# Optimization experiments

Measured on AMD Instinct MI355X. Metric: run time of the kernel, lower is better.

The kernel has to match this reference:

```python
import jax, jax.numpy as jnp
import numpy as np

NUM_HEADS = 8
EPS = 1e-12  # torch F.normalize eps


def setup_inputs() -> dict:
    key = jax.random.key(0)
    k1, k2, k3 = jax.random.split(key, 3)
    B, N, C = 8, 4096, 768
    x = jax.random.normal(k1, (B, N, C), dtype=jnp.float32)
    Wqkv = jax.random.normal(k2, (C, 3 * C), dtype=jnp.float32) * 0.02
    temperature = jnp.ones((NUM_HEADS, 1, 1), dtype=jnp.float32)
    Wproj = jax.random.normal(k3, (C, C), dtype=jnp.float32) * 0.02
    bproj = jnp.zeros((C,), dtype=jnp.float32)
    return {"x": x, "Wqkv": Wqkv, "temperature": temperature,
            "Wproj": Wproj, "bproj": bproj}


def _l2norm(t):
    # torch F.normalize(dim=-1): x / max(||x||, eps)
    n = jnp.sqrt(jnp.sum(t * t, axis=-1, keepdims=True))
    return t / jnp.maximum(n, EPS)


def reference(x, Wqkv, temperature, Wproj, bproj):
    B, N, C = x.shape
    H = NUM_HEADS
    Ch = C // H
    qkv = (x @ Wqkv).reshape(B, N, 3, H, Ch)
    qkv = qkv.transpose(2, 0, 3, 1, 4)           # (3, B, H, N, Ch)
    q, k, v = qkv[0], qkv[1], qkv[2]
    # transpose(-2,-1): attend over channels -> (B, H, Ch, N)
    q = jnp.swapaxes(q, -2, -1)
    k = jnp.swapaxes(k, -2, -1)
    v = jnp.swapaxes(v, -2, -1)
    q = _l2norm(q)
    k = _l2norm(k)
    # (B, H, Ch, Ch) channel-attention scores, scaled by learned temperature
    attn = jnp.einsum('bhcn,bhdn->bhcd', q, k) * temperature
    attn = jax.nn.softmax(attn, axis=-1)
    out = jnp.einsum('bhcd,bhdn->bhcn', attn, v)  # (B, H, Ch, N)
    out = out.transpose(0, 3, 1, 2).reshape(B, N, C)
    return out @ Wproj + bproj
```

## Files before the change

### kernel.cpp

```cpp
#include <hip/hip_runtime.h>
#include <cstdint>
#include <cstddef>

typedef unsigned short u16;
typedef short bf16x8 __attribute__((ext_vector_type(8)));
typedef unsigned short u16x4 __attribute__((ext_vector_type(4)));
typedef unsigned short u16x8 __attribute__((ext_vector_type(8)));
typedef float f32x4 __attribute__((ext_vector_type(4)));

#define EPSN 1e-12f

__device__ __forceinline__ u16 f2bf(float f) {
  uint32_t u = __builtin_bit_cast(uint32_t, f);
  u += 0x7FFFu + ((u >> 16) & 1u);
  return (u16)(u >> 16);
}
__device__ __forceinline__ float bf2f(u16 h) {
  uint32_t u = ((uint32_t)h) << 16;
  return __builtin_bit_cast(float, u);
}

__device__ __forceinline__ void gll16(const u16* g, u16* l) {
  __builtin_amdgcn_global_load_lds(
      (const __attribute__((address_space(1))) void*)g,
      (__attribute__((address_space(3))) void*)l, 16, 0, 0);
}

__global__ __launch_bounds__(256)
void k_cvtT(const float* __restrict__ x, u16* __restrict__ Xh,
            u16* __restrict__ XhT) {
  __shared__ u16 tr[64][68];
  const int tid = threadIdx.x;
  const int t0 = blockIdx.x * 64, k0 = blockIdx.y * 64, b = blockIdx.z;
  const int rq = tid >> 4;
  const int cq = tid & 15;
  const size_t base = ((size_t)b * 4096 + t0) * 768 + k0;
  u16 m[4][4];
#pragma unroll
  for (int e = 0; e < 4; e++) {
    const int r = rq * 4 + e;
    f32x4 v = *(const f32x4*)(x + base + (size_t)r * 768 + cq * 4);
    u16x4 o;
#pragma unroll
    for (int q = 0; q < 4; q++) o[q] = f2bf(v[q]);
    *(u16x4*)(Xh + base + (size_t)r * 768 + cq * 4) = o;
    m[e][0] = o[0]; m[e][1] = o[1]; m[e][2] = o[2]; m[e][3] = o[3];
  }
#pragma unroll
  for (int q = 0; q < 4; q++) {
    u16x4 w;
    w[0] = m[0][q]; w[1] = m[1][q]; w[2] = m[2][q]; w[3] = m[3][q];
    *(u16x4*)&tr[cq * 4 + q][rq * 4] = w;
  }
  __syncthreads();
  const size_t tbase = ((size_t)b * 768 + k0) * 4096 + t0;
#pragma unroll
  for (int p = 0; p < 4; p++) {
    const int kk = (tid >> 4) + p * 16;
    const int ts = (tid & 15) * 4;
    u16x4 o = *(const u16x4*)&tr[kk][ts];
    *(u16x4*)(XhT + tbase + (size_t)kk * 4096 + ts) = o;
  }
}

__global__ __launch_bounds__(256)
void k_wt(const float* __restrict__ W, u16* __restrict__ Wt, u16* __restrict__ Wvh) {
  __shared__ float tile[32][33];
  const int j0 = blockIdx.x * 32;
  const int k0 = blockIdx.y * 32;
  const int tx = threadIdx.x & 31;
  const int ty = threadIdx.x >> 5;
#pragma unroll
  for (int r = 0; r < 4; r++) {
    float v = W[(size_t)(k0 + ty + r * 8) * 2304 + j0 + tx];
    tile[ty + r * 8][tx] = v;
    if (j0 >= 1536)
      Wvh[(size_t)(k0 + ty + r * 8) * 768 + (j0 - 1536) + tx] = f2bf(v);
  }
  __syncthreads();
  if (j0 < 1536) {
#pragma unroll
    for (int r = 0; r < 4; r++)
      Wt[(size_t)(j0 + ty + r * 8) * 768 + k0 + tx] = f2bf(tile[tx][ty + r * 8]);
  }
}

template <int OUTF32B, int TRI>
__global__ __launch_bounds__(256, 3)
void k_gemm(const u16* __restrict__ A, const u16* __restrict__ Btp,
            void* __restrict__ Cp, const float* __restrict__ bias,
            int K, int lda, int ldb, int ldc,
            long aZ, long bZ, long cZ, int zK, long kss) {
  const int gx = gridDim.x, gy = gridDim.y;
  int f = blockIdx.x + gx * (blockIdx.y + gy * blockIdx.z);
  const int total = gx * gy * gridDim.z;
  const int q = total >> 3, rr = total & 7;
  const int xcd = f & 7, kk0 = f >> 3;
  f = (xcd < rr ? xcd * (q + 1) : rr * (q + 1) + (xcd - rr) * q) + kk0;
  const int bx = f % gx;
  const int tmp = f / gx;
  const int by = tmp % gy;
  const int bz = tmp / gy;

  int m0, n0;
  if constexpr (TRI) {
    const int ty = (bx >= 20) ? 5 : (bx >= 18) ? 4 : (bx >= 15) ? 3
                 : (bx >= 11) ? 2 : (bx >= 6) ? 1 : 0;
    const int txi = ty + (bx - (ty * 6 - (ty * (ty - 1)) / 2));
    m0 = ty * 128;
    n0 = txi * 128;
  } else {
    m0 = by * 128;
    n0 = bx * 128;
  }
  const int z = bz;
  const int bb = z / zK, ss = z % zK;
  const u16* Az = A + (long)bb * aZ + (long)ss * kss;
  const u16* Btz = Btp + (long)bb * bZ + (long)ss * kss;

  __shared__ u16 As[3 * 128 * 32];
  __shared__ u16 Bs[3 * 128 * 32];
  const int tid = threadIdx.x;
  const int lane = tid & 63;
  const int wid = tid >> 6;
  const int wr = wid >> 1, wc = wid & 1;
  const int fm = lane & 15, kg = lane >> 4;

  const int lr = lane >> 2;
  const int gk = (lane & 3) ^ ((lane >> 3) & 3);
  const u16* gA = Az + (size_t)(m0 + wid * 32 + lr) * lda + gk * 8;
  const u16* gB = Btz + (size_t)(n0 + wid * 32 + lr) * ldb + gk * 8;
  const size_t a16 = (size_t)16 * lda, b16 = (size_t)16 * ldb;
  u16* lA = As + wid * 1024;
  u16* lB = Bs + wid * 1024;
  const int kq = (kg ^ ((fm >> 1) & 3)) * 8;

  auto STAGE = [&](int slot, int ko) {
    u16* la = lA + slot * 4096;
    u16* lb = lB + slot * 4096;
    gll16(gA + ko, la);
    gll16(gA + ko + a16, la + 512);
    gll16(gB + ko, lb);
    gll16(gB + ko + b16, lb + 512);
  };

  const int nt = K >> 5;
  STAGE(0, 0);
  STAGE(1, 32);
  int sl = 0;

  f32x4 acc[4][4] = {};
  for (int t = 0; t < nt; ++t) {
    if (t + 1 < nt) {
      asm volatile("s_waitcnt vmcnt(4)" ::: "memory");
    } else {
      asm volatile("s_waitcnt vmcnt(0)" ::: "memory");
    }
    __builtin_amdgcn_sched_barrier(0);
    __builtin_amdgcn_s_barrier();
    __builtin_amdgcn_sched_barrier(0);

    if (t + 2 < nt) {
      int s2 = sl + 2; if (s2 >= 3) s2 -= 3;
      STAGE(s2, (t + 2) * 32);
    }

    const u16* as_ = As + sl * 4096;
    const u16* bs_ = Bs + sl * 4096;
    bf16x8 af[4], bfr[4];
#pragma unroll
    for (int i = 0; i < 4; i++)
      af[i] = *(const bf16x8*)&as_[(wr * 64 + i * 16 + fm) * 32 + kq];
#pragma unroll
    for (int j = 0; j < 4; j++)
      bfr[j] = *(const bf16x8*)&bs_[(wc * 64 + j * 16 + fm) * 32 + kq];
    asm volatile("s_waitcnt lgkmcnt(0)" ::: "memory");
    __builtin_amdgcn_sched_barrier(0);

#pragma unroll
    for (int i = 0; i < 4; i++)
#pragma unroll
      for (int j = 0; j < 4; j++)
        acc[i][j] = __builtin_amdgcn_mfma_f32_16x16x32_bf16(af[i], bfr[j], acc[i][j], 0, 0, 0);

    sl++; if (sl == 3) sl = 0;
  }

  if constexpr (OUTF32B) {
    float* C = (float*)Cp + (long)z * cZ;
#pragma unroll
    for (int j = 0; j < 4; j++) {
      const int col = n0 + wc * 64 + j * 16 + fm;
      const float bj = bias[col];
#pragma unroll
      for (int i = 0; i < 4; i++) {
        const int r0 = m0 + wr * 64 + i * 16 + kg * 4;
#pragma unroll
        for (int r = 0; r < 4; r++)
          C[(size_t)(r0 + r) * ldc + col] = acc[i][j][r] + bj;
      }
    }
  } else {
    const int rb = TRI ? 0 : m0;
    const int cb = TRI ? 0 : n0;
    const int ld = TRI ? 128 : ldc;
    u16* C = (u16*)Cp + (long)z * cZ + (TRI ? (long)bx * 16384 : 0L);
#pragma unroll
    for (int j = 0; j < 4; j++) {
      const int col = cb + wc * 64 + j * 16 + fm;
#pragma unroll
      for (int i = 0; i < 4; i++) {
        const int r0 = rb + wr * 64 + i * 16 + kg * 4;
#pragma unroll
        for (int r = 0; r < 4; r++)
          C[(size_t)(r0 + r) * ld + col] = f2bf(acc[i][j][r]);
      }
    }
  }
}

__global__ __launch_bounds__(256)
void k_red(const u16* __restrict__ P, u16* __restrict__ O) {
  const int b = blockIdx.y;
  const int ti = blockIdx.x / 6, tj = blockIdx.x % 6;
  const bool mirror = ti > tj;
  const int a = mirror ? tj : ti;
  const int c2 = mirror ? ti : tj;
  const int src = a * 6 - (a * (a - 1)) / 2 + (c2 - a);
  __shared__ u16 lt[128 * 128];
  const int tid = threadIdx.x;
  const int r = tid >> 1;
  const int ch = (tid & 1) * 64;
  float acc[64] = {};
  for (int s = 0; s < 4; s++) {
    const u16* p = P + ((size_t)(b * 4 + s) * 344064 + (size_t)src * 16384);
    __syncthreads();
#pragma unroll
    for (int it = 0; it < 8; it++) {
      const int idx = (tid + it * 256) * 8;
      *(u16x8*)&lt[idx] = *(const u16x8*)(p + idx);
    }
    __syncthreads();
    if (!mirror) {
#pragma unroll
      for (int e = 0; e < 64; e++) acc[e] += bf2f(lt[r * 128 + ch + e]);
    } else {
#pragma unroll
      for (int e = 0; e < 64; e++) acc[e] += bf2f(lt[(ch + e) * 128 + r]);
    }
  }
  u16* o = O + (size_t)b * 589824 + (size_t)(ti * 128 + r) * 768 + tj * 128 + ch;
#pragma unroll
  for (int v8 = 0; v8 < 8; v8++) {
    u16x8 w;
#pragma unroll
    for (int e = 0; e < 8; e++) w[e] = f2bf(acc[v8 * 8 + e]);
    *(u16x8*)(o + v8 * 8) = w;
  }
}

__global__ __launch_bounds__(256)
void k_score(const u16* __restrict__ Tm, const u16* __restrict__ Wt,
             const float* __restrict__ temperature, float* __restrict__ Aattn) {
  const int h = blockIdx.x, b = blockIdx.y;
  const int bh = b * 8 + h;
  __shared__ u16 As[96 * 32];
  __shared__ u16 Bs[96 * 32];
  __shared__ u16 Dt2[96 * 32];
  __shared__ u16 Dwq[96 * 32];
  __shared__ float Gs[96 * 96];
  __shared__ float nqs[96], nks[96], invk[96];

  const int tid = threadIdx.x;
  const int lane = tid & 63;
  const int wid = tid >> 6;
  const int wr = wid >> 1, wc = wid & 1;
  const int fm = lane & 15, kg = lane >> 4;
  const int lr = lane >> 2;
  const int gkS = (lane & 3) ^ ((lane >> 3) & 3);
  const int gkL = (lane & 3);
  const int kq = (kg ^ ((fm >> 1) & 3)) * 8;

  const u16* baseT1 = Tm + (size_t)b * 1179648 + (size_t)(h * 96) * 768;
  const u16* baseT2 = baseT1 + (size_t)768 * 768;
  const u16* baseWq = Wt + (size_t)(h * 96) * 768;
  const u16* baseWk = baseWq + (size_t)768 * 768;

  const u16* gsrc;
  u16* ldst;
  int gblk = gkS;
  if (wid == 0) { gsrc = baseT1; ldst = As; }
  else if (wid == 1) { gsrc = baseWk; ldst = Bs; }
  else if (wid == 2) { gsrc = baseT2; ldst = Dt2; gblk = gkL; }
  else { gsrc = baseWq; ldst = Dwq; gblk = gkL; }

  f32x4 acc[3][3] = {};
  float nqa = 0.f, nka = 0.f;
  const int sw1 = (tid < 96) ? ((tid >> 1) & 3) : 0;
  const int sw2 = (tid >= 128 && tid < 224) ? (((tid - 128) >> 1) & 3) : 0;

  for (int k0 = 0; k0 < 768; k0 += 32) {
    __syncthreads();
#pragma unroll
    for (int c = 0; c < 6; c++) {
      gll16(gsrc + (size_t)(c * 16 + lr) * 768 + k0 + gblk * 8,
            ldst + c * 512);
    }
    __syncthreads();
    bf16x8 af[3], bfr[3];
#pragma unroll
    for (int i = 0; i < 3; i++)
      af[i] = *(const bf16x8*)&As[(wr * 48 + i * 16 + fm) * 32 + kq];
#pragma unroll
    for (int j = 0; j < 3; j++)
      bfr[j] = *(const bf16x8*)&Bs[(wc * 48 + j * 16 + fm) * 32 + kq];
#pragma unroll
    for (int i = 0; i < 3; i++)
#pragma unroll
      for (int j = 0; j < 3; j++)
        acc[i][j] = __builtin_amdgcn_mfma_f32_16x16x32_bf16(af[i], bfr[j], acc[i][j], 0, 0, 0);
    if (tid < 96) {
#pragma unroll
      for (int g = 0; g < 4; g++) {
        u16x8 av = *(const u16x8*)&As[tid * 32 + (g ^ sw1) * 8];
        u16x8 w = *(const u16x8*)&Dwq[tid * 32 + g * 8];
#pragma unroll
        for (int e = 0; e < 8; e++) nqa += bf2f(av[e]) * bf2f(w[e]);
      }
    } else if (tid >= 128 && tid < 224) {
      const int d = tid - 128;
#pragma unroll
      for (int g = 0; g < 4; g++) {
        u16x8 av = *(const u16x8*)&Bs[d * 32 + (g ^ sw2) * 8];
        u16x8 w = *(const u16x8*)&Dt2[d * 32 + g * 8];
#pragma unroll
        for (int e = 0; e < 8; e++) nka += bf2f(av[e]) * bf2f(w[e]);
      }
    }
  }

  if (tid < 96) nqs[tid] = nqa;
  if (tid >= 128 && tid < 224) nks[tid - 128] = nka;
#pragma unroll
  for (int i = 0; i < 3; i++)
#pragma unroll
    for (int j = 0; j < 3; j++)
#pragma unroll
      for (int r = 0; r < 4; r++)
        Gs[(wr * 48 + i * 16 + kg * 4 + r) * 96 + wc * 48 + j * 16 + fm] = acc[i][j][r];
  __syncthreads();
  if (tid < 96) invk[tid] = 1.0f / fmaxf(sqrtf(nks[tid]), EPSN);
  __syncthreads();
  if (tid < 96) {
    const int c = tid;
    const float iq = temperature[h] / fmaxf(sqrtf(nqs[c]), EPSN);
    float sv[96];
    float m = -1e30f;
#pragma unroll
    for (int d = 0; d < 96; d++) {
      float s = Gs[c * 96 + d] * iq * invk[d];
      sv[d] = s;
      m = fmaxf(m, s);
    }
    float sum = 0.f;
#pragma unroll
    for (int d = 0; d < 96; d++) {
      float e = __expf(sv[d] - m);
      sv[d] = e;
      sum += e;
    }
    const float inv = 1.0f / sum;
    float* dst = Aattn + (size_t)bh * 9216 + (size_t)c * 96;
#pragma unroll
    for (int d = 0; d < 96; d++) dst[d] = sv[d] * inv;
  }
}

__global__ __launch_bounds__(256)
void k_weff(const float* __restrict__ Aattn, const float* __restrict__ Wproj,
            u16* __restrict__ Weff) {
  const int jt = blockIdx.x, h = blockIdx.y, b = blockIdx.z;
  const int bh = b * 8 + h;
  __shared__ float As2[9216];
  const int tid = threadIdx.x;
  for (int idx = tid; idx < 9216; idx += 256)
    As2[idx] = Aattn[(size_t)bh * 9216 + idx];
  __syncthreads();
  const int jloc = tid & 127;
  const int half = tid >> 7;
  const int j = jt * 128 + jloc;
  float acc[48] = {};
  for (int c = 0; c < 96; c++) {
    const float w = Wproj[(size_t)(h * 96 + c) * 768 + j];
    const f32x4* ar = (const f32x4*)&As2[c * 96 + half * 48];
#pragma unroll
    for (int v4 = 0; v4 < 12; v4++) {
      f32x4 av = ar[v4];
      acc[v4 * 4 + 0] += w * av[0];
      acc[v4 * 4 + 1] += w * av[1];
      acc[v4 * 4 + 2] += w * av[2];
      acc[v4 * 4 + 3] += w * av[3];
    }
  }
  u16* dst = Weff + ((size_t)b * 768 + j) * 768 + h * 96 + half * 48;
#pragma unroll
  for (int v4 = 0; v4 < 12; v4++) {
    u16x4 o;
    o[0] = f2bf(acc[v4 * 4 + 0]);
    o[1] = f2bf(acc[v4 * 4 + 1]);
    o[2] = f2bf(acc[v4 * 4 + 2]);
    o[3] = f2bf(acc[v4 * 4 + 3]);
    *(u16x4*)(dst + v4 * 4) = o;
  }
}

extern "C" void kernel_launch(void* const* d_in, const int* in_sizes, int n_in,
                              void* d_out, int out_size, void* d_ws, size_t ws_size,
                              hipStream_t stream) {
  const float* x = (const float*)d_in[0];
  const float* Wqkv = (const float*)d_in[1];
  const float* temp = (const float*)d_in[2];
  const float* Wproj = (const float*)d_in[3];
  const float* bproj = (const float*)d_in[4];
  float* out = (float*)d_out;

  char* ws = (char*)d_ws;
  u16* Xh = (u16*)ws;
  u16* XhT = (u16*)(ws + 50331648);
  u16* Wt = (u16*)(ws + 100663296);
  u16* Wvh = (u16*)(ws + 103022592);
  u16* XtXp = (u16*)(ws + 104202240);
  u16* XtXbf = (u16*)(ws + 141950976);
  u16* T = (u16*)(ws + 151388160);
  u16* WeffT = (u16*)(ws + 151388160);
  u16* WcompT = (u16*)(ws + 160825344);
  float* Aattn = (float*)(ws + 170262528);

  k_cvtT<<<dim3(64, 12, 8), 256, 0, stream>>>(x, Xh, XhT);
  k_wt<<<dim3(72, 24), 256, 0, stream>>>(Wqkv, Wt, Wvh);
  k_gemm<0, 1><<<dim3(21, 1, 32), 256, 0, stream>>>(
      XhT, XhT, (void*)XtXp, nullptr, 1024, 4096, 4096, 0,
      3145728L, 3145728L, 344064L, 4, 1024L);
  k_red<<<dim3(36, 8), 256, 0, stream>>>(XtXp, XtXbf);
  k_gemm<0, 0><<<dim3(6, 12, 8), 256, 0, stream>>>(
      Wt, XtXbf, (void*)T, nullptr, 768, 768, 768, 768,
      0L, 589824L, 1179648L, 1, 0L);
  k_score<<<dim3(8, 8), 256, 0, stream>>>(T, Wt, temp, Aattn);
  k_weff<<<dim3(6, 8, 8), 256, 0, stream>>>(Aattn, Wproj, WeffT);
  k_gemm<0, 0><<<dim3(6, 6, 8), 256, 0, stream>>>(
      WeffT, Wvh, (void*)WcompT, nullptr, 768, 768, 768, 768,
      589824L, 0L, 589824L, 1, 0L);
  k_gemm<1, 0><<<dim3(6, 32, 8), 256, 0, stream>>>(
      Xh, WcompT, out, bproj, 768, 768, 768, 768,
      3145728L, 589824L, 3145728L, 1, 0L);
}
```

Before: 298.3 us.

## Replace LDS-staged GEMM pipeline with direct global-to-register double buffering

After: 507.6 us. +70.1%, slower.

```diff
diff --git a/kernel.cpp b/kernel.cpp
--- a/kernel.cpp
+++ b/kernel.cpp
@@ -118,72 +118,50 @@
   const u16* Az = A + (long)bb * aZ + (long)ss * kss;
   const u16* Btz = Btp + (long)bb * bZ + (long)ss * kss;
 
-  __shared__ u16 As[3 * 128 * 32];
-  __shared__ u16 Bs[3 * 128 * 32];
   const int tid = threadIdx.x;
   const int lane = tid & 63;
   const int wid = tid >> 6;
   const int wr = wid >> 1, wc = wid & 1;
   const int fm = lane & 15, kg = lane >> 4;
 
-  const int lr = lane >> 2;
-  const int gk = (lane & 3) ^ ((lane >> 3) & 3);
-  const u16* gA = Az + (size_t)(m0 + wid * 32 + lr) * lda + gk * 8;
-  const u16* gB = Btz + (size_t)(n0 + wid * 32 + lr) * ldb + gk * 8;
+  const u16* aP = Az + (size_t)(m0 + wr * 64 + fm) * lda + kg * 8;
+  const u16* bP = Btz + (size_t)(n0 + wc * 64 + fm) * ldb + kg * 8;
   const size_t a16 = (size_t)16 * lda, b16 = (size_t)16 * ldb;
-  u16* lA = As + wid * 1024;
-  u16* lB = Bs + wid * 1024;
-  const int kq = (kg ^ ((fm >> 1) & 3)) * 8;
-
-  auto STAGE = [&](int slot, int ko) {
-    u16* la = lA + slot * 4096;
-    u16* lb = lB + slot * 4096;
-    gll16(gA + ko, la);
-    gll16(gA + ko + a16, la + 512);
-    gll16(gB + ko, lb);
-    gll16(gB + ko + b16, lb + 512);
+
+  auto LOADA = [&](bf16x8* d, int ko) {
+#pragma unroll
+    for (int i = 0; i < 4; i++)
+      d[i] = *(const bf16x8*)(aP + (size_t)i * a16 + ko);
   };
+  auto LOADB = [&](bf16x8* d, int ko) {
+#pragma unroll
+    for (int j = 0; j < 4; j++)
+      d[j] = *(const bf16x8*)(bP + (size_t)j * b16 + ko);
+  };
+
+  f32x4 acc[4][4] = {};
+  bf16x8 a0[4], b0[4], a1[4], b1[4];
 
   const int nt = K >> 5;
-  STAGE(0, 0);
-  STAGE(1, 32);
-  int sl = 0;
-
-  f32x4 acc[4][4] = {};
-  for (int t = 0; t < nt; ++t) {
-    if (t + 1 < nt) {
-      asm volatile("s_waitcnt vmcnt(4)" ::: "memory");
-    } else {
-      asm volatile("s_waitcnt vmcnt(0)" ::: "memory");
-    }
-    __builtin_amdgcn_sched_barrier(0);
-    __builtin_amdgcn_s_barrier();
-    __builtin_amdgcn_sched_barrier(0);
-
+  LOADA(a0, 0);
+  LOADB(b0, 0);
+  for (int t = 0; t < nt; t += 2) {
+    LOADA(a1, (t + 1) * 32);
+    LOADB(b1, (t + 1) * 32);
+#pragma unroll
+    for (int i = 0; i < 4; i++)
+#pragma unroll
+      for (int j = 0; j < 4; j++)
+        acc[i][j] = __builtin_amdgcn_mfma_f32_16x16x32_bf16(a0[i], b0[j], acc[i][j], 0, 0, 0);
     if (t + 2 < nt) {
-      int s2 = sl + 2; if (s2 >= 3) s2 -= 3;
-      STAGE(s2, (t + 2) * 32);
-    }
-
-    const u16* as_ = As + sl * 4096;
-    const u16* bs_ = Bs + sl * 4096;
-    bf16x8 af[4], bfr[4];
+      LOADA(a0, (t + 2) * 32);
+      LOADB(b0, (t + 2) * 32);
+    }
 #pragma unroll
     for (int i = 0; i < 4; i++)
-      af[i] = *(const bf16x8*)&as_[(wr * 64 + i * 16 + fm) * 32 + kq];
-#pragma unroll
-    for (int j = 0; j < 4; j++)
-      bfr[j] = *(const bf16x8*)&bs_[(wc * 64 + j * 16 + fm) * 32 + kq];
-    asm volatile("s_waitcnt lgkmcnt(0)" ::: "memory");
-    __builtin_amdgcn_sched_barrier(0);
-
-#pragma unroll
-    for (int i = 0; i < 4; i++)
 #pragma unroll
       for (int j = 0; j < 4; j++)
-        acc[i][j] = __builtin_amdgcn_mfma_f32_16x16x32_bf16(af[i], bfr[j], acc[i][j], 0, 0, 0);
-
-    sl++; if (sl == 3) sl = 0;
+        acc[i][j] = __builtin_amdgcn_mfma_f32_16x16x32_bf16(a1[i], b1[j], acc[i][j], 0, 0, 0);
   }
 
   if constexpr (OUTF32B) {
```

## Reorder GEMM prefetch before wait and add 256x128 8-wave kernel for final projection

Applied to the files above, without the earlier changes.

Result: no change. 301.0 us (median of 3 runs) (+0.9%).

```diff
diff --git a/kernel.cpp b/kernel.cpp
--- a/kernel.cpp
+++ b/kernel.cpp
@@ -147,11 +147,15 @@
   const int nt = K >> 5;
   STAGE(0, 0);
   STAGE(1, 32);
-  int sl = 0;
+  int sC = 0, sN = 1, sS = 2;
 
   f32x4 acc[4][4] = {};
   for (int t = 0; t < nt; ++t) {
-    if (t + 1 < nt) {
+    if (t + 2 < nt) {
+      STAGE(sS, (t + 2) * 32);
+      __builtin_amdgcn_sched_barrier(0);
+      asm volatile("s_waitcnt vmcnt(8)" ::: "memory");
+    } else if (t + 2 == nt) {
       asm volatile("s_waitcnt vmcnt(4)" ::: "memory");
     } else {
       asm volatile("s_waitcnt vmcnt(0)" ::: "memory");
@@ -160,13 +164,8 @@
     __builtin_amdgcn_s_barrier();
     __builtin_amdgcn_sched_barrier(0);
 
-    if (t + 2 < nt) {
-      int s2 = sl + 2; if (s2 >= 3) s2 -= 3;
-      STAGE(s2, (t + 2) * 32);
-    }
-
-    const u16* as_ = As + sl * 4096;
-    const u16* bs_ = Bs + sl * 4096;
+    const u16* as_ = As + sC * 4096;
+    const u16* bs_ = Bs + sC * 4096;
     bf16x8 af[4], bfr[4];
 #pragma unroll
     for (int i = 0; i < 4; i++)
@@ -176,6 +175,8 @@
       bfr[j] = *(const bf16x8*)&bs_[(wc * 64 + j * 16 + fm) * 32 + kq];
     asm volatile("s_waitcnt lgkmcnt(0)" ::: "memory");
     __builtin_amdgcn_sched_barrier(0);
+    __builtin_amdgcn_s_barrier();
+    __builtin_amdgcn_sched_barrier(0);
 
 #pragma unroll
     for (int i = 0; i < 4; i++)
@@ -183,7 +184,7 @@
       for (int j = 0; j < 4; j++)
         acc[i][j] = __builtin_amdgcn_mfma_f32_16x16x32_bf16(af[i], bfr[j], acc[i][j], 0, 0, 0);
 
-    sl++; if (sl == 3) sl = 0;
+    const int t2 = sC; sC = sN; sN = sS; sS = t2;
   }
 
   if constexpr (OUTF32B) {
@@ -214,6 +215,103 @@
 #pragma unroll
         for (int r = 0; r < 4; r++)
           C[(size_t)(r0 + r) * ld + col] = f2bf(acc[i][j][r]);
+      }
+    }
+  }
+}
+
+template <int OUTF32B>
+__global__ __launch_bounds__(512, 4)
+void k_gemm2(const u16* __restrict__ A, const u16* __restrict__ Btp,
+             void* __restrict__ Cp, const float* __restrict__ bias,
+             int K, int lda, int ldb, int ldc,
+             long aZ, long bZ, long cZ) {
+  const int gx = gridDim.x, gy = gridDim.y;
+  int f = blockIdx.x + gx * (blockIdx.y + gy * blockIdx.z);
+  const int total = gx * gy * gridDim.z;
+  const int q = total >> 3, rr = total & 7;
+  const int xcd = f & 7, kk0 = f >> 3;
+  f = (xcd < rr ? xcd * (q + 1) : rr * (q + 1) + (xcd - rr) * q) + kk0;
+  const int bx = f % gx;
+  const int tmp = f / gx;
+  const int by = tmp % gy;
+  const int bz = tmp / gy;
+
+  const int m0 = by * 256, n0 = bx * 128;
+  const u16* Az = A + (long)bz * aZ;
+  const u16* Btz = Btp + (long)bz * bZ;
+
+  __shared__ u16 As[2][256 * 32];
+  __shared__ u16 Bs[2][128 * 32];
+  const int tid = threadIdx.x;
+  const int lane = tid & 63;
+  const int wid = tid >> 6;
+  const int wr = wid & 3, wc = wid >> 2;
+  const int fm = lane & 15, kg = lane >> 4;
+
+  const int lr = lane >> 2;
+  const int gk = (lane & 3) ^ ((lane >> 3) & 3);
+  const u16* gA = Az + (size_t)(m0 + wid * 32 + lr) * lda + gk * 8;
+  const u16* gB = Btz + (size_t)(n0 + wid * 16 + lr) * ldb + gk * 8;
+  const size_t a16 = (size_t)16 * lda;
+  const int kq = (kg ^ ((fm >> 1) & 3)) * 8;
+
+  auto STAGE = [&](int s, int ko) {
+    u16* la = &As[s][wid * 1024];
+    u16* lb = &Bs[s][wid * 512];
+    gll16(gA + ko, la);
+    gll16(gA + ko + a16, la + 512);
+    gll16(gB + ko, lb);
+  };
+
+  const int nt = K >> 5;
+  STAGE(0, 0);
+  int cur = 0;
+
+  f32x4 acc[4][4] = {};
+  for (int t = 0; t < nt; ++t) {
+    __syncthreads();
+    bf16x8 af[4], bfr[4];
+#pragma unroll
+    for (int i = 0; i < 4; i++)
+      af[i] = *(const bf16x8*)&As[cur][(wr * 64 + i * 16 + fm) * 32 + kq];
+#pragma unroll
+    for (int j = 0; j < 4; j++)
+      bfr[j] = *(const bf16x8*)&Bs[cur][(wc * 64 + j * 16 + fm) * 32 + kq];
+    if (t + 1 < nt) STAGE(cur ^ 1, (t + 1) * 32);
+#pragma unroll
+    for (int i = 0; i < 4; i++)
+#pragma unroll
+      for (int j = 0; j < 4; j++)
+        acc[i][j] = __builtin_amdgcn_mfma_f32_16x16x32_bf16(af[i], bfr[j], acc[i][j], 0, 0, 0);
+    cur ^= 1;
+  }
+
+  if constexpr (OUTF32B) {
+    float* C = (float*)Cp + (long)bz * cZ;
+#pragma unroll
+    for (int j = 0; j < 4; j++) {
+      const int col = n0 + wc * 64 + j * 16 + fm;
+      const float bj = bias[col];
+#pragma unroll
+      for (int i = 0; i < 4; i++) {
+        const int r0 = m0 + wr * 64 + i * 16 + kg * 4;
+#pragma unroll
+        for (int r = 0; r < 4; r++)
+          C[(size_t)(r0 + r) * ldc + col] = acc[i][j][r] + bj;
+      }
+    }
+  } else {
+    u16* C = (u16*)Cp + (long)bz * cZ;
+#pragma unroll
+    for (int j = 0; j < 4; j++) {
+      const int col = n0 + wc * 64 + j * 16 + fm;
+#pragma unroll
+      for (int i = 0; i < 4; i++) {
+        const int r0 = m0 + wr * 64 + i * 16 + kg * 4;
+#pragma unroll
+        for (int r = 0; r < 4; r++)
+          C[(size_t)(r0 + r) * ldc + col] = f2bf(acc[i][j][r]);
       }
     }
   }
@@ -450,7 +548,7 @@
   k_gemm<0, 0><<<dim3(6, 6, 8), 256, 0, stream>>>(
       WeffT, Wvh, (void*)WcompT, nullptr, 768, 768, 768, 768,
       589824L, 0L, 589824L, 1, 0L);
-  k_gemm<1, 0><<<dim3(6, 32, 8), 256, 0, stream>>>(
+  k_gemm2<1><<<dim3(6, 16, 8), 512, 0, stream>>>(
       Xh, WcompT, out, bproj, 768, 768, 768, 768,
-      3145728L, 589824L, 3145728L, 1, 0L);
-}
+      3145728L, 589824L, 3145728L);
+}
```
